# Kernel tuning notes

Measured on AMD Instinct MI355X. Metric: run time of the kernel, lower is better.

The kernel has to match this reference:

```python
import jax, jax.numpy as jnp
import numpy as np
import math

NUM_HEADS = 16
D_MODEL = 1024
LN_EPS = 1e-5


def _layer_norm(x, g, b):
    mu = jnp.mean(x, axis=-1, keepdims=True)
    var = jnp.mean((x - mu) ** 2, axis=-1, keepdims=True)
    return (x - mu) / jnp.sqrt(var + LN_EPS) * g + b


def setup_inputs() -> dict:
    key = jax.random.key(0)
    ks = jax.random.split(key, 12)
    B, H, W, d = 32, 16, 16, D_MODEL
    P, F = 64, 128
    s = 0.02
    return {
        "x": jax.random.normal(ks[0], (B, H, W, d), jnp.float32),
        "pattern_features": jax.random.normal(ks[1], (B, P, F), jnp.float32),
        "wq": jax.random.normal(ks[2], (d, d), jnp.float32) * s,
        "bq": jnp.zeros((d,), jnp.float32),
        "wk": jax.random.normal(ks[3], (d, d), jnp.float32) * s,
        "bk": jnp.zeros((d,), jnp.float32),
        "wv": jax.random.normal(ks[4], (d, d), jnp.float32) * s,
        "bv": jnp.zeros((d,), jnp.float32),
        "wo": jax.random.normal(ks[5], (d, d), jnp.float32) * s,
        "bo": jnp.zeros((d,), jnp.float32),
        "ln_g": jnp.ones((d,), jnp.float32),
        "ln_b": jnp.zeros((d,), jnp.float32),
    }


def reference(x, pattern_features, wq, bq, wk, bk, wv, bv, wo, bo, ln_g, ln_b):
    B, H, W, d = x.shape
    S = H * W
    nh = NUM_HEADS
    dk = d // nh
    x_seq = x.reshape(B, S, d)

    def proj(w, b):
        return (x_seq @ w.T + b).reshape(B, S, nh, dk).transpose(0, 2, 1, 3)  # (B,nh,S,dk)

    q, k, v = proj(wq, bq), proj(wk, bk), proj(wv, bv)
    scores = jnp.einsum("bhsd,bhtd->bhst", q, k) / math.sqrt(dk)  # (B,nh,S,S)

    # creative bias: diversity bonus on top-left min(S,64) block, same for all heads
    m = min(S, 64)
    sim = jnp.einsum("bpf,bqf->bpq", pattern_features, pattern_features)
    div = 1.0 - jax.nn.softmax(sim, axis=-1)  # (B,P,P)
    bias = jnp.zeros((B, nh, S, S), x.dtype)
    bias = bias.at[:, :, :m, :m].set(div[:, None, :m, :m] * 0.1)

    # faithful to torch: scores + bias.unsqueeze(0) -> rank-5 (1,B,nh,S,S)
    scores5 = scores[None] + bias[None]
    aw = jax.nn.softmax(scores5, axis=-1)
    attn = jnp.matmul(aw, v)  # (1,B,nh,S,dk) via broadcasting
    # faithful to torch transpose(1,2).view(B,S,d): row-major reshape of (1,nh,B,S,dk)
    attn = jnp.transpose(attn, (0, 2, 1, 3, 4)).reshape(B, S, d)

    out = attn @ wo.T + bo
    out = _layer_norm(out + x_seq, ln_g, ln_b)

    attention_weights = jax.nn.softmax(scores, axis=-1).mean(axis=1)  # (B,S,S)
    return out.reshape(B, H, W, d), attention_weights
```

## Files before the change

kernel.cpp:

```cpp
#include <hip/hip_runtime.h>

typedef unsigned short u16;
typedef unsigned int   u32;
typedef short bf16x8 __attribute__((ext_vector_type(8)));
typedef float f32x4  __attribute__((ext_vector_type(4)));

__device__ __forceinline__ float bf2f(u16 u){
  union { u32 u; float f; } c; c.u = ((u32)u) << 16; return c.f;
}
__device__ __forceinline__ u16 f2bf(float f){
  union { float f; u32 u; } c; c.f = f;
  u32 u = c.u + 0x7fffu + ((c.u >> 16) & 1u);
  return (u16)(u >> 16);
}

__device__ __forceinline__ void gload16(const u16* g, u16* l){
  __builtin_amdgcn_global_load_lds((const __attribute__((address_space(1))) u32*)g,
                                   (__attribute__((address_space(3))) u32*)l, 16, 0, 0);
}

__device__ __forceinline__ float waveRed(float v, int ismax){
  #pragma unroll
  for (int o = 32; o > 0; o >>= 1){
    float t = __shfl_xor(v, o, 64);
    v = ismax ? fmaxf(v, t) : (v + t);
  }
  return v;
}
__device__ __forceinline__ float blockRed(float v, int ismax, float* red, int tid){
  v = waveRed(v, ismax);
  __syncthreads();
  if ((tid & 63) == 0) red[tid >> 6] = v;
  __syncthreads();
  return ismax ? fmaxf(fmaxf(red[0], red[1]), fmaxf(red[2], red[3]))
               : (red[0] + red[1] + red[2] + red[3]);
}

__global__ __launch_bounds__(256)
void conv_all(const float* __restrict__ x, const float* __restrict__ w0,
              const float* __restrict__ w1, const float* __restrict__ w2,
              const float* __restrict__ w3, u16* __restrict__ xdst,
              u16* __restrict__ wdst){
  const int bid = blockIdx.x;
  const float* s;
  u16* d;
  size_t i;
  if (bid < 4096){
    s = x; d = xdst;
    i = ((size_t)bid * 256 + threadIdx.x) * 8;
  } else {
    const int wb = bid - 4096;
    const int wi = wb >> 9;
    s = wi == 0 ? w0 : (wi == 1 ? w1 : (wi == 2 ? w2 : w3));
    d = wdst + (size_t)wi * 1048576;
    i = ((size_t)(wb & 511) * 256 + threadIdx.x) * 8;
  }
  const float4 a = *(const float4*)(s + i);
  const float4 b = *(const float4*)(s + i + 4);
  uint4 o;
  o.x = (u32)f2bf(a.x) | ((u32)f2bf(a.y) << 16);
  o.y = (u32)f2bf(a.z) | ((u32)f2bf(a.w) << 16);
  o.z = (u32)f2bf(b.x) | ((u32)f2bf(b.y) << 16);
  o.w = (u32)f2bf(b.z) | ((u32)f2bf(b.w) << 16);
  *(uint4*)(d + i) = o;
}

__global__ __launch_bounds__(256)
void div_kernel(const float* __restrict__ pf, float* __restrict__ divp)
{
  __shared__ float pfs[64][129];
  __shared__ float svs[64][65];
  const int b = blockIdx.x;
  const int tid = threadIdx.x;
  const float* pb = pf + (size_t)b * 8192;
  for (int i = tid; i < 8192; i += 256) pfs[i >> 7][i & 127] = pb[i];
  __syncthreads();
  const int p = tid & 63, qg = tid >> 6;
  for (int qq = qg * 16; qq < qg * 16 + 16; ++qq){
    float a = 0.f;
    #pragma unroll 8
    for (int f = 0; f < 128; ++f) a += pfs[p][f] * pfs[qq][f];
    svs[p][qq] = a;
  }
  __syncthreads();
  if (tid < 64){
    float m = -1e30f;
    for (int qq = 0; qq < 64; ++qq) m = fmaxf(m, svs[tid][qq]);
    float s = 0.f;
    for (int qq = 0; qq < 64; ++qq){ const float e = __expf(svs[tid][qq] - m); svs[tid][qq] = e; s += e; }
    const float inv = 1.f / s;
    float* dr = divp + ((size_t)b * 64 + tid) * 64;
    for (int qq = 0; qq < 64; ++qq) dr[qq] = 0.1f * (1.f - svs[tid][qq] * inv);
  }
}

template<int MODE>
__global__ __launch_bounds__(256, 3)
void gemm_lds(const u16* __restrict__ A, const u16* __restrict__ Wb,
              const float* __restrict__ bias0, const float* __restrict__ bias1,
              const float* __restrict__ bias2, void* __restrict__ outp)
{
  __shared__ u16 As[3][4096];
  __shared__ u16 Bs[3][4096];
  const int tid = threadIdx.x, lane = tid & 63, w = tid >> 6;
  const int wm = (w >> 1) * 64, wn = (w & 1) * 64;
  const int bm = blockIdx.x;
  int bn = blockIdx.y;
  const u16* Wp = Wb;
  const float* bias = bias0;
  float scale = 1.f;
  int wsel = 0;
  if (MODE == 0){
    wsel = bn >> 3; bn &= 7;
    Wp = Wb + (size_t)wsel * 1048576;
    bias = wsel == 0 ? bias0 : (wsel == 1 ? bias1 : bias2);
    if (wsel == 0) scale = 0.125f;
  }

  const f32x4 z = {0.f, 0.f, 0.f, 0.f};
  f32x4 acc[4][4];
  #pragma unroll
  for (int i = 0; i < 4; ++i)
    #pragma unroll
    for (int j = 0; j < 4; ++j) acc[i][j] = z;

  const int r4  = lane >> 2;
  const int c8s = (((lane & 3) ^ ((lane >> 3) & 3)) * 8);
  const int ca0 = w * 2, ca1 = w * 2 + 1;
  const u16* gA0 = A  + (size_t)(bm * 128 + ca0 * 16 + r4) * 1024 + c8s;
  const u16* gA1 = A  + (size_t)(bm * 128 + ca1 * 16 + r4) * 1024 + c8s;
  const u16* gB0 = Wp + (size_t)(bn * 128 + ca0 * 16 + r4) * 1024 + c8s;
  const u16* gB1 = Wp + (size_t)(bn * 128 + ca1 * 16 + r4) * 1024 + c8s;
  const int lo0 = ca0 * 512 + lane * 8;
  const int lo1 = ca1 * 512 + lane * 8;

  const int fr = lane & 15, quad = lane >> 4;
  int offA[4], offB[4];
  #pragma unroll
  for (int i = 0; i < 4; ++i){
    const int r = wm + i * 16 + fr;
    offA[i] = r * 32 + ((quad ^ ((r >> 1) & 3)) * 8);
  }
  #pragma unroll
  for (int j = 0; j < 4; ++j){
    const int r = wn + j * 16 + fr;
    offB[j] = r * 32 + ((quad ^ ((r >> 1) & 3)) * 8);
  }

#define STG(s, kk) \
    gload16(gA0 + (kk), &As[s][lo0]); \
    gload16(gA1 + (kk), &As[s][lo1]); \
    gload16(gB0 + (kk), &Bs[s][lo0]); \
    gload16(gB1 + (kk), &Bs[s][lo1]);

  STG(0, 0)
  STG(1, 32)
  asm volatile("s_waitcnt vmcnt(4)" ::: "memory");
  __builtin_amdgcn_sched_barrier(0);
  __builtin_amdgcn_s_barrier();
  asm volatile("" ::: "memory");
  __builtin_amdgcn_sched_barrier(0);

  int slot = 0;
  #pragma unroll 1
  for (int t = 0; t < 32; ++t){
    const int s2 = slot < 1 ? 2 : slot - 1;
    if (t < 30){ STG(s2, (t + 2) * 32) }
    const u16* as_ = As[slot];
    const u16* bs_ = Bs[slot];
    bf16x8 af[4], bfv[4];
    #pragma unroll
    for (int i = 0; i < 4; ++i) af[i]  = *(const bf16x8*)&as_[offA[i]];
    #pragma unroll
    for (int j = 0; j < 4; ++j) bfv[j] = *(const bf16x8*)&bs_[offB[j]];
    __builtin_amdgcn_s_setprio(1);
    #pragma unroll
    for (int i = 0; i < 4; ++i)
      #pragma unroll
      for (int j = 0; j < 4; ++j)
        acc[i][j] = __builtin_amdgcn_mfma_f32_16x16x32_bf16(af[i], bfv[j], acc[i][j], 0, 0, 0);
    __builtin_amdgcn_s_setprio(0);
    if (t < 30)       { asm volatile("s_waitcnt vmcnt(4)" ::: "memory"); }
    else if (t == 30) { asm volatile("s_waitcnt vmcnt(0)" ::: "memory"); }
    if (t < 31){
      __builtin_amdgcn_sched_barrier(0);
      __builtin_amdgcn_s_barrier();
      asm volatile("" ::: "memory");
      __builtin_amdgcn_sched_barrier(0);
    }
    slot = slot == 2 ? 0 : slot + 1;
  }
#undef STG

  #pragma unroll
  for (int i = 0; i < 4; ++i){
    #pragma unroll
    for (int j = 0; j < 4; ++j){
      const int gr0 = bm * 128 + wm + i * 16 + quad * 4;
      const int gc  = bn * 128 + wn + j * 16 + fr;
      const float bvv = bias[gc];
      if (MODE == 0 && wsel == 2){
        const int b = gr0 >> 8, s0 = gr0 & 255, h = gc >> 6, kk = gc & 63;
        const u32 p0 = (u32)f2bf(acc[i][j][0] + bvv) |
                       ((u32)f2bf(acc[i][j][1] + bvv) << 16);
        const u32 p1 = (u32)f2bf(acc[i][j][2] + bvv) |
                       ((u32)f2bf(acc[i][j][3] + bvv) << 16);
        uint2 pk; pk.x = p0; pk.y = p1;
        *(uint2*)((u16*)outp + (size_t)2 * 8388608 + (size_t)b * 262144 +
                  (size_t)h * 16384 + (size_t)kk * 256 + s0) = pk;
      } else {
        #pragma unroll
        for (int r = 0; r < 4; ++r){
          const int gr = gr0 + r;
          const float val = (acc[i][j][r] + bvv) * scale;
          if (MODE == 0){
            const int b = gr >> 8, s = gr & 255, h = gc >> 6, kk = gc & 63;
            ((u16*)outp)[(size_t)wsel * 8388608 + (size_t)b * 262144 +
                         (size_t)h * 16384 + (size_t)s * 64 + kk] = f2bf(val);
          } else {
            ((float*)outp)[(size_t)gr * 1024 + gc] = val;
          }
        }
      }
    }
  }
}

__global__ __launch_bounds__(256)
void attn_mfma(const u16* __restrict__ q, const u16* __restrict__ k,
               const u16* __restrict__ vT, const float* __restrict__ divp,
               u16* __restrict__ attn_s)
{
  __shared__ u16 Ps[4][16][136];
  const int bh = blockIdx.x;
  const int b = bh >> 4, h = bh & 15;
  const int tid = threadIdx.x, lane = tid & 63, w = tid >> 6;
  const int quad = lane >> 4, l15 = lane & 15;
  const u16* kh = k  + (size_t)bh * 16384;
  const u16* vh = vT + (size_t)bh * 16384;
  const u16* qh = q  + (size_t)bh * 16384;

  const f32x4 z = {0.f, 0.f, 0.f, 0.f};
  const int bp = 2 * h + (b >> 4);
  for (int i = 0; i < 4; ++i){
    const int row0 = w * 64 + i * 16;
    const bf16x8 af0 = *(const bf16x8*)(qh + (size_t)(row0 + l15) * 64 + quad * 8);
    const bf16x8 af1 = *(const bf16x8*)(qh + (size_t)(row0 + l15) * 64 + 32 + quad * 8);
    f32x4 sc[16];
    #pragma unroll
    for (int ct = 0; ct < 16; ++ct){
      const bf16x8 b0 = *(const bf16x8*)(kh + (size_t)(ct * 16 + l15) * 64 + quad * 8);
      const bf16x8 b1 = *(const bf16x8*)(kh + (size_t)(ct * 16 + l15) * 64 + 32 + quad * 8);
      f32x4 a = __builtin_amdgcn_mfma_f32_16x16x32_bf16(af0, b0, z, 0, 0, 0);
      sc[ct]  = __builtin_amdgcn_mfma_f32_16x16x32_bf16(af1, b1, a, 0, 0, 0);
    }
    if (w == 0){
      const float* dv = divp + (size_t)b * 4096 + (size_t)(i * 16 + quad * 4) * 64 + l15;
      #pragma unroll
      for (int ct = 0; ct < 4; ++ct)
        #pragma unroll
        for (int rr = 0; rr < 4; ++rr)
          sc[ct][rr] += dv[rr * 64 + ct * 16];
    }
    float rs[4];
    #pragma unroll
    for (int rr = 0; rr < 4; ++rr){
      float m = sc[0][rr];
      #pragma unroll
      for (int ct = 1; ct < 16; ++ct) m = fmaxf(m, sc[ct][rr]);
      #pragma unroll
      for (int o = 1; o < 16; o <<= 1) m = fmaxf(m, __shfl_xor(m, o, 64));
      float s = 0.f;
      #pragma unroll
      for (int ct = 0; ct < 16; ++ct){
        const float e = __expf(sc[ct][rr] - m); sc[ct][rr] = e; s += e;
      }
      #pragma unroll
      for (int o = 1; o < 16; o <<= 1) s += __shfl_xor(s, o, 64);
      rs[rr] = 1.f / s;
    }
    f32x4 o4[4] = {z, z, z, z};
    #pragma unroll
    for (int half = 0; half < 2; ++half){
      #pragma unroll
      for (int ct = 0; ct < 8; ++ct)
        #pragma unroll
        for (int rr = 0; rr < 4; ++rr)
          Ps[w][quad * 4 + rr][ct * 16 + l15] = f2bf(sc[half * 8 + ct][rr] * rs[rr]);
      #pragma unroll
      for (int kc = 0; kc < 4; ++kc){
        const bf16x8 pa = *(const bf16x8*)&Ps[w][l15][kc * 32 + quad * 8];
        #pragma unroll
        for (int nt = 0; nt < 4; ++nt){
          const bf16x8 vb8 = *(const bf16x8*)(vh + (size_t)(nt * 16 + l15) * 256 +
                                              half * 128 + kc * 32 + quad * 8);
          o4[nt] = __builtin_amdgcn_mfma_f32_16x16x32_bf16(pa, vb8, o4[nt], 0, 0, 0);
        }
      }
    }
    const int sp = (b & 15) * 16 + (w * 4 + i);
    #pragma unroll
    for (int nt = 0; nt < 4; ++nt)
      #pragma unroll
      for (int rr = 0; rr < 4; ++rr){
        const int slo = quad * 4 + rr;
        const int cp = slo * 64 + nt * 16 + l15;
        attn_s[((size_t)bp * 256 + sp) * 1024 + cp] = f2bf(o4[nt][rr]);
      }
  }
}

__global__ __launch_bounds__(256)
void aw_kernel(const u16* __restrict__ q, const u16* __restrict__ k,
               float* __restrict__ aw)
{
  __shared__ __align__(16) float awl[4][16][260];
  const int blk = blockIdx.x;
  const int b = blk >> 4, st = blk & 15;
  const int tid = threadIdx.x, lane = tid & 63, w = tid >> 6;
  const int quad = lane >> 4, l15 = lane & 15;
  const int rowb = st * 16;
  const f32x4 z = {0.f, 0.f, 0.f, 0.f};
  float awacc[16][4] = {};
  #pragma unroll 1
  for (int hi = 0; hi < 4; ++hi){
    const int h = hi * 4 + w;
    const u16* kh = k + (((size_t)b * 16 + h) * 16384);
    const u16* qh = q + (((size_t)b * 16 + h) * 16384);
    const bf16x8 af0 = *(const bf16x8*)(qh + (size_t)(rowb + l15) * 64 + quad * 8);
    const bf16x8 af1 = *(const bf16x8*)(qh + (size_t)(rowb + l15) * 64 + 32 + quad * 8);
    f32x4 sc[16];
    #pragma unroll
    for (int ct = 0; ct < 16; ++ct){
      const bf16x8 b0 = *(const bf16x8*)(kh + (size_t)(ct * 16 + l15) * 64 + quad * 8);
      const bf16x8 b1 = *(const bf16x8*)(kh + (size_t)(ct * 16 + l15) * 64 + 32 + quad * 8);
      f32x4 a = __builtin_amdgcn_mfma_f32_16x16x32_bf16(af0, b0, z, 0, 0, 0);
      sc[ct]  = __builtin_amdgcn_mfma_f32_16x16x32_bf16(af1, b1, a, 0, 0, 0);
    }
    #pragma unroll
    for (int rr = 0; rr < 4; ++rr){
      float m = sc[0][rr];
      #pragma unroll
      for (int ct = 1; ct < 16; ++ct) m = fmaxf(m, sc[ct][rr]);
      #pragma unroll
      for (int o = 1; o < 16; o <<= 1) m = fmaxf(m, __shfl_xor(m, o, 64));
      float s = 0.f;
      #pragma unroll
      for (int ct = 0; ct < 16; ++ct){
        const float e = __expf(sc[ct][rr] - m); sc[ct][rr] = e; s += e;
      }
      #pragma unroll
      for (int o = 1; o < 16; o <<= 1) s += __shfl_xor(s, o, 64);
      const float inv = 1.f / s;
      #pragma unroll
      for (int ct = 0; ct < 16; ++ct) awacc[ct][rr] += sc[ct][rr] * inv;
    }
  }
  #pragma unroll
  for (int ct = 0; ct < 16; ++ct)
    #pragma unroll
    for (int rr = 0; rr < 4; ++rr)
      awl[w][quad * 4 + rr][ct * 16 + l15] = awacc[ct][rr];
  __syncthreads();
  const size_t base = (size_t)b * 65536 + (size_t)rowb * 256;
  #pragma unroll
  for (int cc = 0; cc < 4; ++cc){
    const int idx = cc * 1024 + tid * 4;
    const int row = idx >> 8, col = idx & 255;
    const float4 a0 = *(const float4*)&awl[0][row][col];
    const float4 a1 = *(const float4*)&awl[1][row][col];
    const float4 a2 = *(const float4*)&awl[2][row][col];
    const float4 a3 = *(const float4*)&awl[3][row][col];
    float4 o;
    o.x = (a0.x + a1.x + a2.x + a3.x) * 0.0625f;
    o.y = (a0.y + a1.y + a2.y + a3.y) * 0.0625f;
    o.z = (a0.z + a1.z + a2.z + a3.z) * 0.0625f;
    o.w = (a0.w + a1.w + a2.w + a3.w) * 0.0625f;
    *(float4*)(aw + base + idx) = o;
  }
}

__global__ __launch_bounds__(256)
void ln_kernel(const float* __restrict__ y2, const float* __restrict__ x,
               const float* __restrict__ g, const float* __restrict__ bb,
               float* __restrict__ outp)
{
  __shared__ float red[4];
  const int r = blockIdx.x, tid = threadIdx.x;
  const float4 yv = ((const float4*)(y2 + (size_t)r * 1024))[tid];
  const float4 xv = ((const float4*)(x  + (size_t)r * 1024))[tid];
  const float v0 = yv.x + xv.x;
  const float v1 = yv.y + xv.y;
  const float v2 = yv.z + xv.z;
  const float v3 = yv.w + xv.w;
  const float ssum = blockRed(v0 + v1 + v2 + v3, 0, red, tid);
  const float mu = ssum * (1.f / 1024.f);
  const float d0 = v0 - mu, d1 = v1 - mu, d2 = v2 - mu, d3 = v3 - mu;
  const float sq = blockRed(d0 * d0 + d1 * d1 + d2 * d2 + d3 * d3, 0, red, tid);
  const float rstd = rsqrtf(sq * (1.f / 1024.f) + 1e-5f);
  const float4 gv = ((const float4*)g)[tid];
  const float4 bv = ((const float4*)bb)[tid];
  float4 o;
  o.x = d0 * rstd * gv.x + bv.x;
  o.y = d1 * rstd * gv.y + bv.y;
  o.z = d2 * rstd * gv.z + bv.z;
  o.w = d3 * rstd * gv.w + bv.w;
  ((float4*)(outp + (size_t)r * 1024))[tid] = o;
}

extern "C" void kernel_launch(void* const* d_in, const int* in_sizes, int n_in,
                              void* d_out, int out_size, void* d_ws, size_t ws_size,
                              hipStream_t stream)
{
  int ix = -1, ipf = -1, iw[4] = {-1,-1,-1,-1}, iv[6] = {-1,-1,-1,-1,-1,-1};
  int nw = 0, nv = 0;
  for (int i = 0; i < n_in; ++i){
    const int sz = in_sizes[i];
    if (sz == 8388608 && ix < 0) ix = i;
    else if (sz == 262144 && ipf < 0) ipf = i;
    else if (sz == 1048576 && nw < 4) iw[nw++] = i;
    else if (sz == 1024 && nv < 6) iv[nv++] = i;
  }
  if (ix < 0 || ipf < 0 || nw != 4 || nv != 6){
    ix = 0; ipf = 1; iw[0] = 2; iv[0] = 3; iw[1] = 4; iv[1] = 5;
    iw[2] = 6; iv[2] = 7; iw[3] = 8; iv[3] = 9; iv[4] = 10; iv[5] = 11;
  }

  const float* x   = (const float*)d_in[ix];
  const float* pf  = (const float*)d_in[ipf];
  const float* wq  = (const float*)d_in[iw[0]];
  const float* wk  = (const float*)d_in[iw[1]];
  const float* wv  = (const float*)d_in[iw[2]];
  const float* wo  = (const float*)d_in[iw[3]];
  const float* bq  = (const float*)d_in[iv[0]];
  const float* bk  = (const float*)d_in[iv[1]];
  const float* bv  = (const float*)d_in[iv[2]];
  const float* bo  = (const float*)d_in[iv[3]];
  const float* lng = (const float*)d_in[iv[4]];
  const float* lnb = (const float*)d_in[iv[5]];

  float* out0   = (float*)d_out;
  float* aw_out = out0 + 8388608;

  u16* x_bf = (u16*)d_out;
  u16* attn = x_bf + 8388608;
  u16* qkv    = (u16*)d_ws;
  float* divp = (float*)((char*)d_ws + (size_t)48 * 1048576);
  u16* warena = (u16*)((char*)d_ws + (size_t)49 * 1048576);
  float* y2   = (float*)d_ws;

  conv_all<<<6144, 256, 0, stream>>>(x, wq, wk, wv, wo, x_bf, warena);
  div_kernel<<<32, 256, 0, stream>>>(pf, divp);

  gemm_lds<0><<<dim3(64, 24), 256, 0, stream>>>(x_bf, warena, bq, bk, bv, (void*)qkv);

  u16* qw = qkv, *kw = qkv + 8388608, *vw = qkv + 16777216;
  attn_mfma<<<512, 256, 0, stream>>>(qw, kw, vw, divp, attn);
  aw_kernel<<<512, 256, 0, stream>>>(qw, kw, aw_out);

  gemm_lds<1><<<dim3(64, 8), 256, 0, stream>>>(attn, warena + 3145728, bo, nullptr, nullptr, (void*)y2);
  ln_kernel<<<8192, 256, 0, stream>>>(y2, x, lng, lnb, out0);
}
```

Baseline: 339.1 us.

## Fuse attention and head-averaged weights kernels; swap operands for V transpose store

Merges the attention-output kernel and the head-mean attention-weights kernel into one kernel that computes QK^T once per (batch, row-tile, head) and derives both the unbiased softmax average and the biased softmax for PV. This removes the duplicated QK^T matmuls and the extra read of Q and K. The V projection GEMM now swaps its operands, so the transposed V layout is written directly by row. Blocks are also remapped in interleaved order. The risks are extra exp work in the bias-tile blocks, higher register pressure from the awacc array under a 2-wave occupancy hint, and scalar 2-byte stores in the V epilogue.

Result: faster. 325.3 us (-4.1%).

```diff
diff --git a/kernel.cpp b/kernel.cpp
--- a/kernel.cpp
+++ b/kernel.cpp
@@ -116,6 +116,11 @@
     bias = wsel == 0 ? bias0 : (wsel == 1 ? bias1 : bias2);
     if (wsel == 0) scale = 0.125f;
   }
+  const bool vsw = (MODE == 0 && wsel == 2);
+  const int mt  = vsw ? bn : bm;
+  const int nt2 = vsw ? bm : bn;
+  const u16* MA = vsw ? Wp : A;
+  const u16* MB = vsw ? A  : Wp;
 
   const f32x4 z = {0.f, 0.f, 0.f, 0.f};
   f32x4 acc[4][4];
@@ -127,10 +132,10 @@
   const int r4  = lane >> 2;
   const int c8s = (((lane & 3) ^ ((lane >> 3) & 3)) * 8);
   const int ca0 = w * 2, ca1 = w * 2 + 1;
-  const u16* gA0 = A  + (size_t)(bm * 128 + ca0 * 16 + r4) * 1024 + c8s;
-  const u16* gA1 = A  + (size_t)(bm * 128 + ca1 * 16 + r4) * 1024 + c8s;
-  const u16* gB0 = Wp + (size_t)(bn * 128 + ca0 * 16 + r4) * 1024 + c8s;
-  const u16* gB1 = Wp + (size_t)(bn * 128 + ca1 * 16 + r4) * 1024 + c8s;
+  const u16* gA0 = MA + (size_t)(mt  * 128 + ca0 * 16 + r4) * 1024 + c8s;
+  const u16* gA1 = MA + (size_t)(mt  * 128 + ca1 * 16 + r4) * 1024 + c8s;
+  const u16* gB0 = MB + (size_t)(nt2 * 128 + ca0 * 16 + r4) * 1024 + c8s;
+  const u16* gB1 = MB + (size_t)(nt2 * 128 + ca1 * 16 + r4) * 1024 + c8s;
   const int lo0 = ca0 * 512 + lane * 8;
   const int lo1 = ca1 * 512 + lane * 8;
 
@@ -196,19 +201,20 @@
   for (int i = 0; i < 4; ++i){
     #pragma unroll
     for (int j = 0; j < 4; ++j){
-      const int gr0 = bm * 128 + wm + i * 16 + quad * 4;
-      const int gc  = bn * 128 + wn + j * 16 + fr;
-      const float bvv = bias[gc];
-      if (MODE == 0 && wsel == 2){
-        const int b = gr0 >> 8, s0 = gr0 & 255, h = gc >> 6, kk = gc & 63;
-        const u32 p0 = (u32)f2bf(acc[i][j][0] + bvv) |
-                       ((u32)f2bf(acc[i][j][1] + bvv) << 16);
-        const u32 p1 = (u32)f2bf(acc[i][j][2] + bvv) |
-                       ((u32)f2bf(acc[i][j][3] + bvv) << 16);
-        uint2 pk; pk.x = p0; pk.y = p1;
-        *(uint2*)((u16*)outp + (size_t)2 * 8388608 + (size_t)b * 262144 +
-                  (size_t)h * 16384 + (size_t)kk * 256 + s0) = pk;
+      const int gr0 = mt  * 128 + wm + i * 16 + quad * 4;
+      const int gc  = nt2 * 128 + wn + j * 16 + fr;
+      if (vsw){
+        const int bb = gc >> 8, s = gc & 255;
+        #pragma unroll
+        for (int r = 0; r < 4; ++r){
+          const int grow = gr0 + r;
+          const int h = grow >> 6, kk = grow & 63;
+          ((u16*)outp)[(size_t)2 * 8388608 + (size_t)bb * 262144 +
+                       (size_t)h * 16384 + (size_t)kk * 256 + s] =
+            f2bf(acc[i][j][r] + bias[grow]);
+        }
       } else {
+        const float bvv = bias[gc];
         #pragma unroll
         for (int r = 0; r < 4; ++r){
           const int gr = gr0 + r;
@@ -226,26 +232,29 @@
   }
 }
 
-__global__ __launch_bounds__(256)
-void attn_mfma(const u16* __restrict__ q, const u16* __restrict__ k,
-               const u16* __restrict__ vT, const float* __restrict__ divp,
-               u16* __restrict__ attn_s)
+__global__ __launch_bounds__(256, 2)
+void attn_aw(const u16* __restrict__ q, const u16* __restrict__ k,
+             const u16* __restrict__ vT, const float* __restrict__ divp,
+             u16* __restrict__ attn_s, float* __restrict__ aw)
 {
-  __shared__ u16 Ps[4][16][136];
-  const int bh = blockIdx.x;
-  const int b = bh >> 4, h = bh & 15;
+  __shared__ __align__(16) u16 Ps[4][16][136];
+  const int raw = blockIdx.x;
+  const int blk = (raw & 7) * 64 + (raw >> 3);
+  const int b = blk >> 4, st = blk & 15;
   const int tid = threadIdx.x, lane = tid & 63, w = tid >> 6;
   const int quad = lane >> 4, l15 = lane & 15;
-  const u16* kh = k  + (size_t)bh * 16384;
-  const u16* vh = vT + (size_t)bh * 16384;
-  const u16* qh = q  + (size_t)bh * 16384;
-
+  const int rowb = st * 16;
   const f32x4 z = {0.f, 0.f, 0.f, 0.f};
-  const int bp = 2 * h + (b >> 4);
-  for (int i = 0; i < 4; ++i){
-    const int row0 = w * 64 + i * 16;
-    const bf16x8 af0 = *(const bf16x8*)(qh + (size_t)(row0 + l15) * 64 + quad * 8);
-    const bf16x8 af1 = *(const bf16x8*)(qh + (size_t)(row0 + l15) * 64 + 32 + quad * 8);
+  float awacc[16][4] = {};
+
+  #pragma unroll 1
+  for (int hi = 0; hi < 4; ++hi){
+    const int h = hi * 4 + w;
+    const u16* qh = q  + ((size_t)b * 16 + h) * 16384;
+    const u16* kh = k  + ((size_t)b * 16 + h) * 16384;
+    const u16* vh = vT + ((size_t)b * 16 + h) * 16384;
+    const bf16x8 af0 = *(const bf16x8*)(qh + (size_t)(rowb + l15) * 64 + quad * 8);
+    const bf16x8 af1 = *(const bf16x8*)(qh + (size_t)(rowb + l15) * 64 + 32 + quad * 8);
     f32x4 sc[16];
     #pragma unroll
     for (int ct = 0; ct < 16; ++ct){
@@ -254,30 +263,67 @@
       f32x4 a = __builtin_amdgcn_mfma_f32_16x16x32_bf16(af0, b0, z, 0, 0, 0);
       sc[ct]  = __builtin_amdgcn_mfma_f32_16x16x32_bf16(af1, b1, a, 0, 0, 0);
     }
-    if (w == 0){
-      const float* dv = divp + (size_t)b * 4096 + (size_t)(i * 16 + quad * 4) * 64 + l15;
+    float rs[4];
+    if (st < 4){
+      #pragma unroll
+      for (int rr = 0; rr < 4; ++rr){
+        float m = sc[0][rr];
+        #pragma unroll
+        for (int ct = 1; ct < 16; ++ct) m = fmaxf(m, sc[ct][rr]);
+        #pragma unroll
+        for (int o = 1; o < 16; o <<= 1) m = fmaxf(m, __shfl_xor(m, o, 64));
+        float s = 0.f;
+        #pragma unroll
+        for (int ct = 0; ct < 16; ++ct) s += __expf(sc[ct][rr] - m);
+        #pragma unroll
+        for (int o = 1; o < 16; o <<= 1) s += __shfl_xor(s, o, 64);
+        const float inv = 1.f / s;
+        #pragma unroll
+        for (int ct = 0; ct < 16; ++ct)
+          awacc[ct][rr] += __expf(sc[ct][rr] - m) * inv;
+      }
+      const float* dv = divp + (size_t)b * 4096 + (size_t)(rowb + quad * 4) * 64 + l15;
       #pragma unroll
       for (int ct = 0; ct < 4; ++ct)
         #pragma unroll
         for (int rr = 0; rr < 4; ++rr)
           sc[ct][rr] += dv[rr * 64 + ct * 16];
-    }
-    float rs[4];
-    #pragma unroll
-    for (int rr = 0; rr < 4; ++rr){
-      float m = sc[0][rr];
-      #pragma unroll
-      for (int ct = 1; ct < 16; ++ct) m = fmaxf(m, sc[ct][rr]);
-      #pragma unroll
-      for (int o = 1; o < 16; o <<= 1) m = fmaxf(m, __shfl_xor(m, o, 64));
-      float s = 0.f;
-      #pragma unroll
-      for (int ct = 0; ct < 16; ++ct){
-        const float e = __expf(sc[ct][rr] - m); sc[ct][rr] = e; s += e;
+      #pragma unroll
+      for (int rr = 0; rr < 4; ++rr){
+        float m = sc[0][rr];
+        #pragma unroll
+        for (int ct = 1; ct < 16; ++ct) m = fmaxf(m, sc[ct][rr]);
+        #pragma unroll
+        for (int o = 1; o < 16; o <<= 1) m = fmaxf(m, __shfl_xor(m, o, 64));
+        float s = 0.f;
+        #pragma unroll
+        for (int ct = 0; ct < 16; ++ct){
+          const float e = __expf(sc[ct][rr] - m); sc[ct][rr] = e; s += e;
+        }
+        #pragma unroll
+        for (int o = 1; o < 16; o <<= 1) s += __shfl_xor(s, o, 64);
+        rs[rr] = 1.f / s;
       }
-      #pragma unroll
-      for (int o = 1; o < 16; o <<= 1) s += __shfl_xor(s, o, 64);
-      rs[rr] = 1.f / s;
+    } else {
+      #pragma unroll
+      for (int rr = 0; rr < 4; ++rr){
+        float m = sc[0][rr];
+        #pragma unroll
+        for (int ct = 1; ct < 16; ++ct) m = fmaxf(m, sc[ct][rr]);
+        #pragma unroll
+        for (int o = 1; o < 16; o <<= 1) m = fmaxf(m, __shfl_xor(m, o, 64));
+        float s = 0.f;
+        #pragma unroll
+        for (int ct = 0; ct < 16; ++ct){
+          const float e = __expf(sc[ct][rr] - m); sc[ct][rr] = e; s += e;
+        }
+        #pragma unroll
+        for (int o = 1; o < 16; o <<= 1) s += __shfl_xor(s, o, 64);
+        rs[rr] = 1.f / s;
+        #pragma unroll
+        for (int ct = 0; ct < 16; ++ct)
+          awacc[ct][rr] += sc[ct][rr] * rs[rr];
+      }
     }
     f32x4 o4[4] = {z, z, z, z};
     #pragma unroll
@@ -298,85 +344,37 @@
         }
       }
     }
-    const int sp = (b & 15) * 16 + (w * 4 + i);
+    const size_t rbase = ((size_t)(512 * h + 16 * b + st)) * 1024;
     #pragma unroll
     for (int nt = 0; nt < 4; ++nt)
       #pragma unroll
-      for (int rr = 0; rr < 4; ++rr){
-        const int slo = quad * 4 + rr;
-        const int cp = slo * 64 + nt * 16 + l15;
-        attn_s[((size_t)bp * 256 + sp) * 1024 + cp] = f2bf(o4[nt][rr]);
-      }
-  }
-}
-
-__global__ __launch_bounds__(256)
-void aw_kernel(const u16* __restrict__ q, const u16* __restrict__ k,
-               float* __restrict__ aw)
-{
-  __shared__ __align__(16) float awl[4][16][260];
-  const int blk = blockIdx.x;
-  const int b = blk >> 4, st = blk & 15;
-  const int tid = threadIdx.x, lane = tid & 63, w = tid >> 6;
-  const int quad = lane >> 4, l15 = lane & 15;
-  const int rowb = st * 16;
-  const f32x4 z = {0.f, 0.f, 0.f, 0.f};
-  float awacc[16][4] = {};
-  #pragma unroll 1
-  for (int hi = 0; hi < 4; ++hi){
-    const int h = hi * 4 + w;
-    const u16* kh = k + (((size_t)b * 16 + h) * 16384);
-    const u16* qh = q + (((size_t)b * 16 + h) * 16384);
-    const bf16x8 af0 = *(const bf16x8*)(qh + (size_t)(rowb + l15) * 64 + quad * 8);
-    const bf16x8 af1 = *(const bf16x8*)(qh + (size_t)(rowb + l15) * 64 + 32 + quad * 8);
-    f32x4 sc[16];
-    #pragma unroll
-    for (int ct = 0; ct < 16; ++ct){
-      const bf16x8 b0 = *(const bf16x8*)(kh + (size_t)(ct * 16 + l15) * 64 + quad * 8);
-      const bf16x8 b1 = *(const bf16x8*)(kh + (size_t)(ct * 16 + l15) * 64 + 32 + quad * 8);
-      f32x4 a = __builtin_amdgcn_mfma_f32_16x16x32_bf16(af0, b0, z, 0, 0, 0);
-      sc[ct]  = __builtin_amdgcn_mfma_f32_16x16x32_bf16(af1, b1, a, 0, 0, 0);
-    }
-    #pragma unroll
-    for (int rr = 0; rr < 4; ++rr){
-      float m = sc[0][rr];
-      #pragma unroll
-      for (int ct = 1; ct < 16; ++ct) m = fmaxf(m, sc[ct][rr]);
-      #pragma unroll
-      for (int o = 1; o < 16; o <<= 1) m = fmaxf(m, __shfl_xor(m, o, 64));
-      float s = 0.f;
-      #pragma unroll
-      for (int ct = 0; ct < 16; ++ct){
-        const float e = __expf(sc[ct][rr] - m); sc[ct][rr] = e; s += e;
-      }
-      #pragma unroll
-      for (int o = 1; o < 16; o <<= 1) s += __shfl_xor(s, o, 64);
-      const float inv = 1.f / s;
-      #pragma unroll
-      for (int ct = 0; ct < 16; ++ct) awacc[ct][rr] += sc[ct][rr] * inv;
-    }
-  }
-  #pragma unroll
-  for (int ct = 0; ct < 16; ++ct)
-    #pragma unroll
-    for (int rr = 0; rr < 4; ++rr)
-      awl[w][quad * 4 + rr][ct * 16 + l15] = awacc[ct][rr];
-  __syncthreads();
+      for (int rr = 0; rr < 4; ++rr)
+        attn_s[rbase + (size_t)(quad * 4 + rr) * 64 + nt * 16 + l15] = f2bf(o4[nt][rr]);
+  }
+
+  float* awl = (float*)&Ps[0][0][0];
   const size_t base = (size_t)b * 65536 + (size_t)rowb * 256;
   #pragma unroll
   for (int cc = 0; cc < 4; ++cc){
-    const int idx = cc * 1024 + tid * 4;
-    const int row = idx >> 8, col = idx & 255;
-    const float4 a0 = *(const float4*)&awl[0][row][col];
-    const float4 a1 = *(const float4*)&awl[1][row][col];
-    const float4 a2 = *(const float4*)&awl[2][row][col];
-    const float4 a3 = *(const float4*)&awl[3][row][col];
+    __syncthreads();
+    #pragma unroll
+    for (int j = 0; j < 4; ++j)
+      #pragma unroll
+      for (int rr = 0; rr < 4; ++rr)
+        awl[(w * 16 + quad * 4 + rr) * 68 + j * 16 + l15] = awacc[cc * 4 + j][rr];
+    __syncthreads();
+    const int idx = tid * 4;
+    const int row = idx >> 6, col = idx & 63;
+    const float4 a0 = *(const float4*)&awl[(      row) * 68 + col];
+    const float4 a1 = *(const float4*)&awl[(16  + row) * 68 + col];
+    const float4 a2 = *(const float4*)&awl[(32  + row) * 68 + col];
+    const float4 a3 = *(const float4*)&awl[(48  + row) * 68 + col];
     float4 o;
     o.x = (a0.x + a1.x + a2.x + a3.x) * 0.0625f;
     o.y = (a0.y + a1.y + a2.y + a3.y) * 0.0625f;
     o.z = (a0.z + a1.z + a2.z + a3.z) * 0.0625f;
     o.w = (a0.w + a1.w + a2.w + a3.w) * 0.0625f;
-    *(float4*)(aw + base + idx) = o;
+    *(float4*)(aw + base + (size_t)row * 256 + cc * 64 + col) = o;
   }
 }
 
@@ -455,8 +453,7 @@
   gemm_lds<0><<<dim3(64, 24), 256, 0, stream>>>(x_bf, warena, bq, bk, bv, (void*)qkv);
 
   u16* qw = qkv, *kw = qkv + 8388608, *vw = qkv + 16777216;
-  attn_mfma<<<512, 256, 0, stream>>>(qw, kw, vw, divp, attn);
-  aw_kernel<<<512, 256, 0, stream>>>(qw, kw, aw_out);
+  attn_aw<<<512, 256, 0, stream>>>(qw, kw, vw, divp, attn, aw_out);
 
   gemm_lds<1><<<dim3(64, 8), 256, 0, stream>>>(attn, warena + 3145728, bo, nullptr, nullptr, (void*)y2);
   ln_kernel<<<8192, 256, 0, stream>>>(y2, x, lng, lnb, out0);
```
